# Optimization experiments

Hardware: AMD Instinct MI355X
Metric: run time of the kernel (lower is better)

The kernel has to match this reference:

```python
import jax, jax.numpy as jnp
import numpy as np
from jax import lax


def _lstm(x, h, c, W, U, b):
    # torch LSTM gate order: i, f, g, o; b = b_ih + b_hh combined
    g = x @ W.T + h @ U.T + b
    i, f, gg, o = jnp.split(g, 4, axis=-1)
    c2 = jax.nn.sigmoid(f) * c + jax.nn.sigmoid(i) * jnp.tanh(gg)
    h2 = jax.nn.sigmoid(o) * jnp.tanh(c2)
    return h2, c2


def _run_dir(x, mask, W, U, b):
    # packed-sequence semantics: state updates only where mask, outputs 0 at pad
    B = x.shape[0]
    Hh = U.shape[1]
    h0 = jnp.zeros((B, Hh), x.dtype)

    def step(carry, inp):
        h, c = carry
        xt, mt = inp
        h2, c2 = _lstm(xt, h, c, W, U, b)
        m = mt[:, None]
        h = jnp.where(m, h2, h)
        c = jnp.where(m, c2, c)
        return (h, c), jnp.where(m, h, jnp.zeros_like(h))

    (hf, cf), outs = lax.scan(step, (h0, h0), (jnp.swapaxes(x, 0, 1), mask.T))
    return jnp.swapaxes(outs, 0, 1), hf, cf  # (B,S,H), (B,H), (B,H)


def _forward(source, source_mask, target, target_mask, emb_src, emb_tgt,
             eW0f, eU0f, eb0f, eW0b, eU0b, eb0b,
             eW1f, eU1f, eb1f, eW1b, eU1b, eb1b,
             dW0, dU0, db0, dW1, dU1, db1, wW, wb):
    x = emb_src[source]  # (B,S,D)
    finals_h, finals_c = [], []
    enc_params = [(eW0f, eU0f, eb0f, eW0b, eU0b, eb0b),
                  (eW1f, eU1f, eb1f, eW1b, eU1b, eb1b)]
    for Wf, Uf, bf, Wb, Ub, bb in enc_params:
        of, hf, cf = _run_dir(x, source_mask, Wf, Uf, bf)
        # backward direction: reverse time; prefix mask becomes suffix, so the
        # masked-update scan exactly reproduces packed reverse-direction LSTM
        ob, hb, cb = _run_dir(x[:, ::-1], source_mask[:, ::-1], Wb, Ub, bb)
        ob = ob[:, ::-1]
        x = jnp.concatenate([of, ob], axis=-1)
        finals_h.append(jnp.concatenate([hf, hb], axis=-1))  # (B, 2H)
        finals_c.append(jnp.concatenate([cf, cb], axis=-1))

    # decoder initial state: per-layer concat of fwd/bwd encoder final states
    xt = emb_tgt[target]  # (B,T,D)

    def dstep(carry, inp):
        h1, c1, h2, c2 = carry
        t, mt = inp
        m = mt[:, None]
        nh1, nc1 = _lstm(t, h1, c1, dW0, dU0, db0)
        h1 = jnp.where(m, nh1, h1)
        c1 = jnp.where(m, nc1, c1)
        nh2, nc2 = _lstm(h1, h2, c2, dW1, dU1, db1)
        h2 = jnp.where(m, nh2, h2)
        c2 = jnp.where(m, nc2, c2)
        return (h1, c1, h2, c2), jnp.where(m, h2, jnp.zeros_like(h2))

    init = (finals_h[0], finals_c[0], finals_h[1], finals_c[1])
    _, outs = lax.scan(dstep, init, (jnp.swapaxes(xt, 0, 1), target_mask.T))
    outs = jnp.swapaxes(outs, 0, 1)  # (B,T,d_out)
    return jnp.einsum('btd,vd->btv', outs, wW) + wb  # (B,T,V)


def setup_inputs() -> dict:
    key = jax.random.key(0)
    ks = jax.random.split(key, 32)
    B, S, T, V, D, H = 32, 64, 65, 32000, 256, 512
    DO = 2 * H

    def p(i, shape):
        return jax.random.normal(ks[i], shape, dtype=jnp.float32) * 0.05

    source = jax.random.randint(ks[0], (B, S), 0, V + 1)
    target = jax.random.randint(ks[1], (B, T), 0, V + 1)
    # descending-sorted lengths -> sort/perm in the original is identity
    slen = jnp.sort(jax.random.randint(ks[2], (B,), 1, S + 1))[::-1]
    tlen = jnp.sort(jax.random.randint(ks[3], (B,), 1, T + 1))[::-1]
    source_mask = jnp.arange(S)[None, :] < slen[:, None]
    target_mask = jnp.arange(T)[None, :] < tlen[:, None]
    emb = p(4, (V + 1, D))
    return dict(
        source=source, source_mask=source_mask, target=target, target_mask=target_mask,
        emb_src=emb, emb_tgt=emb + 0.0,
        eW0f=p(5, (4 * H, D)), eU0f=p(6, (4 * H, H)), eb0f=p(7, (4 * H,)),
        eW0b=p(8, (4 * H, D)), eU0b=p(9, (4 * H, H)), eb0b=p(10, (4 * H,)),
        eW1f=p(11, (4 * H, 2 * H)), eU1f=p(12, (4 * H, H)), eb1f=p(13, (4 * H,)),
        eW1b=p(14, (4 * H, 2 * H)), eU1b=p(15, (4 * H, H)), eb1b=p(16, (4 * H,)),
        dW0=p(17, (4 * DO, D)), dU0=p(18, (4 * DO, DO)), db0=p(19, (4 * DO,)),
        dW1=p(20, (4 * DO, DO)), dU1=p(21, (4 * DO, DO)), db1=p(22, (4 * DO,)),
        wW=p(23, (V, DO)), wb=p(24, (V,)))


def reference(source, source_mask, target, target_mask, emb_src, emb_tgt,
              eW0f, eU0f, eb0f, eW0b, eU0b, eb0b,
              eW1f, eU1f, eb1f, eW1b, eU1b, eb1b,
              dW0, dU0, db0, dW1, dU1, db1, wW, wb):
    return _forward(source, source_mask, target, target_mask, emb_src, emb_tgt,
                    eW0f, eU0f, eb0f, eW0b, eU0b, eb0b,
                    eW1f, eU1f, eb1f, eW1b, eU1b, eb1b,
                    dW0, dU0, db0, dW1, dU1, db1, wW, wb)
```

## Files before the change

### kernel.cpp

```cpp
#include <hip/hip_runtime.h>

#define B_ 32
#define S_ 64
#define T_ 65
#define D_ 256
#define HE 512
#define HD 1024
#define VV 32000

typedef __attribute__((ext_vector_type(8))) short bf16x8;
typedef __attribute__((ext_vector_type(4))) float f32x4;
typedef __attribute__((ext_vector_type(4))) unsigned int u32x4;

__device__ inline unsigned short f2bf(float f) {
  unsigned int u = __float_as_uint(f);
  u += 0x7FFFu + ((u >> 16) & 1u);
  return (unsigned short)(u >> 16);
}
__device__ inline float sigmf(float x) { return 1.0f / (1.0f + __expf(-x)); }

#define MFMA16(a,b,c) __builtin_amdgcn_mfma_f32_16x16x32_bf16((a),(b),(c),0,0,0)

#define SLOT_STRIDE 32
__device__ inline void gbar_all(int* slots, int nblk, int e, int bid) {
  asm volatile("s_waitcnt vmcnt(0)" ::: "memory");
  __syncthreads();
  const int tid = threadIdx.x;
  if (tid == 0)
    __hip_atomic_store(&slots[bid * SLOT_STRIDE], e, __ATOMIC_RELAXED,
                       __HIP_MEMORY_SCOPE_AGENT);
  if (tid < nblk) {
    while (__hip_atomic_load(&slots[tid * SLOT_STRIDE], __ATOMIC_RELAXED,
                             __HIP_MEMORY_SCOPE_AGENT) < e)
      __builtin_amdgcn_s_sleep(2);
  }
  __syncthreads();
}

__device__ inline u32x4 ld16_sc(const void* p) {
  u32x4 r;
  asm volatile("global_load_dwordx4 %0, %1, off sc1"
               : "=v"(r)
               : "v"((unsigned long long)p)
               : "memory");
  return r;
}

__device__ inline int swz(int row, int col, int LD) {
  return row * LD + ((((col >> 3) ^ (row & 7)) << 3) | (col & 7));
}
template <int LD>
__device__ inline void stage1a(short* lds, const short* src) {
  const int tid = threadIdx.x;
  constexpr int NPT = LD / 64;
  u32x4 t[NPT];
#pragma unroll
  for (int i = 0; i < NPT; i++)
    t[i] = ld16_sc(src + ((size_t)(i * 256 + tid)) * 8);
  asm volatile("s_waitcnt vmcnt(0)" ::: "memory");
  __builtin_amdgcn_sched_barrier(0);
#pragma unroll
  for (int i = 0; i < NPT; i++) {
    int o = (i * 256 + tid) * 8;
    *(u32x4*)(lds + swz(o / LD, o % LD, LD)) = t[i];
  }
}
__device__ inline void stage2a(short* lds1, const short* s1, short* lds2,
                               const short* s2) {
  const int tid = threadIdx.x;
#pragma unroll
  for (int h = 0; h < 2; h++) {
    u32x4 a[8], b[8];
#pragma unroll
    for (int i = 0; i < 8; i++)
      a[i] = ld16_sc(s1 + ((size_t)((h * 8 + i) * 256 + tid)) * 8);
#pragma unroll
    for (int i = 0; i < 8; i++)
      b[i] = ld16_sc(s2 + ((size_t)((h * 8 + i) * 256 + tid)) * 8);
    asm volatile("s_waitcnt vmcnt(0)" ::: "memory");
    __builtin_amdgcn_sched_barrier(0);
#pragma unroll
    for (int i = 0; i < 8; i++) {
      int o = ((h * 8 + i) * 256 + tid) * 8;
      *(u32x4*)(lds1 + swz(o / HD, o % HD, HD)) = a[i];
    }
#pragma unroll
    for (int i = 0; i < 8; i++) {
      int o = ((h * 8 + i) * 256 + tid) * 8;
      *(u32x4*)(lds2 + swz(o / HD, o % HD, HD)) = b[i];
    }
  }
}

__device__ inline int mask_dtype(const unsigned char* m) {
  unsigned b0 = m[0], b1 = m[1], b2 = m[2], b3 = m[3], b4 = m[4];
  if (b0 == 1 && b1 == 1) return 0;
  if (b0 == 1) {
    if (b4 == 1) return 1;
    if (b4 == 0 && m[8] == 1) return 2;
    return 1;
  }
  if (b0 == 0x80 && b1 == 0x3F) return 4;
  if (b0 == 0x00 && b1 == 0x3C) return 5;
  if (b2 == 0x80 && b3 == 0x3F) return 3;
  return 1;
}
__device__ inline int mask_val(const unsigned char* m, int dt, int i) {
  switch (dt) {
    case 0: return m[i] != 0;
    case 1: return ((const int*)m)[i] != 0;
    case 2: return ((const long long*)m)[i] != 0;
    case 3: return ((const float*)m)[i] != 0.0f;
    default: return ((const unsigned short*)m)[i] != 0;
  }
}
__global__ void k_masks(const unsigned char* msrc, const unsigned char* mtgt,
                        signed char* o_src, signed char* o_tgt) {
  const unsigned char* m = blockIdx.x ? mtgt : msrc;
  signed char* o = blockIdx.x ? o_tgt : o_src;
  int n = blockIdx.x ? (B_ * T_) : (B_ * S_);
  int dt = mask_dtype(m);
  for (int i = threadIdx.x; i < n; i += blockDim.x)
    o[i] = (signed char)mask_val(m, dt, i);
}

struct CvtJobs {
  const float* src[13];
  short* dst[13];
  int n4[13];
};
__global__ __launch_bounds__(256) void k_convert(CvtJobs jb) {
  int j = blockIdx.y;
  const float4* s = (const float4*)jb.src[j];
  ushort4* d = (ushort4*)jb.dst[j];
  int n4 = jb.n4[j];
  for (int i = blockIdx.x * blockDim.x + threadIdx.x; i < n4;
       i += gridDim.x * blockDim.x) {
    float4 v = s[i];
    ushort4 o;
    o.x = f2bf(v.x); o.y = f2bf(v.y); o.z = f2bf(v.z); o.w = f2bf(v.w);
    d[i] = o;
  }
}

__global__ __launch_bounds__(256) void k_gather(const int* sids, const int* tids,
                                                const float* es, const float* et,
                                                short* Xs, short* Xt) {
  int job = blockIdx.y;
  int rows = job ? (B_ * T_) : (B_ * S_);
  const int* ids = job ? tids : sids;
  const float* emb = job ? et : es;
  ushort4* X = (ushort4*)(job ? Xt : Xs);
  int total = rows * (D_ / 4);
  for (int i = blockIdx.x * blockDim.x + threadIdx.x; i < total;
       i += gridDim.x * blockDim.x) {
    int row = i >> 6;
    int c4 = i & 63;
    long id = ids[row];
    float4 v = ((const float4*)(emb + id * (long)D_))[c4];
    ushort4 o;
    o.x = f2bf(v.x); o.y = f2bf(v.y); o.z = f2bf(v.z); o.w = f2bf(v.w);
    X[(long)row * 64 + c4] = o;
  }
}

template <bool B_F32, bool C_F32>
__global__ __launch_bounds__(256) void k_gemm(const short* __restrict__ A,
                                              const short* __restrict__ Bw,
                                              const float* __restrict__ Bwf,
                                              const float* __restrict__ bias,
                                              short* __restrict__ C,
                                              float* __restrict__ Cf,
                                              int M_out, int N, int K) {
  __shared__ short As[128 * 32];
  __shared__ short Bs[128 * 32];
  const int tid = threadIdx.x;
  const int wave = tid >> 6, lane = tid & 63;
  const int wm = wave >> 1, wn = wave & 1;
  const int r16 = lane & 15, kb = lane >> 4;
  const long m0 = (long)blockIdx.y * 128;
  const long n0 = (long)blockIdx.x * 128;

  const int ch0 = tid * 2, ch1 = ch0 + 1;
  const int ar0 = ch0 >> 2, ak0 = (ch0 & 3) * 8;
  const int ar1 = ch1 >> 2, ak1 = (ch1 & 3) * 8;

  f32x4 acc[4][4];
#pragma unroll
  for (int i = 0; i < 4; i++)
#pragma unroll
    for (int j = 0; j < 4; j++) acc[i][j] = (f32x4){0.f, 0.f, 0.f, 0.f};

  for (int kt = 0; kt < K; kt += 32) {
    bf16x8 va0 = *(const bf16x8*)(A + (m0 + ar0) * K + kt + ak0);
    bf16x8 va1 = *(const bf16x8*)(A + (m0 + ar1) * K + kt + ak1);
    bf16x8 vb0, vb1;
    if (B_F32) {
      const float* p0 = Bwf + (n0 + ar0) * K + kt + ak0;
      const float* p1 = Bwf + (n0 + ar1) * K + kt + ak1;
      float4 x0 = *(const float4*)p0, x1 = *(const float4*)(p0 + 4);
      float4 y0 = *(const float4*)p1, y1 = *(const float4*)(p1 + 4);
      vb0 = (bf16x8){(short)f2bf(x0.x), (short)f2bf(x0.y), (short)f2bf(x0.z),
                     (short)f2bf(x0.w), (short)f2bf(x1.x), (short)f2bf(x1.y),
                     (short)f2bf(x1.z), (short)f2bf(x1.w)};
      vb1 = (bf16x8){(short)f2bf(y0.x), (short)f2bf(y0.y), (short)f2bf(y0.z),
                     (short)f2bf(y0.w), (short)f2bf(y1.x), (short)f2bf(y1.y),
                     (short)f2bf(y1.z), (short)f2bf(y1.w)};
    } else {
      vb0 = *(const bf16x8*)(Bw + (n0 + ar0) * K + kt + ak0);
      vb1 = *(const bf16x8*)(Bw + (n0 + ar1) * K + kt + ak1);
    }
    __syncthreads();
    *(bf16x8*)(As + ar0 * 32 + ak0) = va0;
    *(bf16x8*)(As + ar1 * 32 + ak1) = va1;
    *(bf16x8*)(Bs + ar0 * 32 + ak0) = vb0;
    *(bf16x8*)(Bs + ar1 * 32 + ak1) = vb1;
    __syncthreads();
    bf16x8 av[4], bv[4];
#pragma unroll
    for (int i = 0; i < 4; i++)
      av[i] = *(const bf16x8*)(As + (wm * 64 + i * 16 + r16) * 32 + kb * 8);
#pragma unroll
    for (int j = 0; j < 4; j++)
      bv[j] = *(const bf16x8*)(Bs + (wn * 64 + j * 16 + r16) * 32 + kb * 8);
#pragma unroll
    for (int i = 0; i < 4; i++)
#pragma unroll
      for (int j = 0; j < 4; j++) acc[i][j] = MFMA16(av[i], bv[j], acc[i][j]);
  }
#pragma unroll
  for (int j = 0; j < 4; j++) {
    long gc = n0 + wn * 64 + j * 16 + r16;
    float bb = bias ? bias[gc] : 0.f;
#pragma unroll
    for (int i = 0; i < 4; i++) {
      long gr0 = m0 + wm * 64 + i * 16 + kb * 4;
#pragma unroll
      for (int r = 0; r < 4; r++) {
        long gr = gr0 + r;
        if (gr < M_out) {
          if (C_F32) Cf[gr * N + gc] = acc[i][j][r] + bb;
          else C[gr * N + gc] = (short)f2bf(acc[i][j][r] + bb);
        }
      }
    }
  }
}

__global__ __launch_bounds__(256) void k_enc_persist(
    const short* __restrict__ Wf, const short* __restrict__ Wb_,
    short* __restrict__ H, const float* __restrict__ Pf,
    const float* __restrict__ Pb, short* __restrict__ Outb, int outLD,
    int outOffDir, float* __restrict__ Cfin,
    const signed char* __restrict__ msk, int* slots) {
  const int dir = blockIdx.y;
  const short* W = dir ? Wb_ : Wf;
  const float* P = dir ? Pb : Pf;
  int* slotsD = slots + dir * 32 * SLOT_STRIDE;
  const int q = threadIdx.x >> 6, lane = threadIdx.x & 63;
  const int r16 = lane & 15, kb = lane >> 4;
  const int n = q * HE + blockIdx.x * 16 + r16;
  const short* wr = W + (size_t)n * HE;
  const int bb = threadIdx.x >> 3;
  const int cp = threadIdx.x & 7;
  const int j0 = blockIdx.x * 16 + 2 * cp;
  __shared__ short h_lds[32 * HE];
  __shared__ float g_lds[4][2][16][17];
  float creg0 = 0.f, creg1 = 0.f;

  for (int s = 0; s < S_; ++s) {
    const int t = dir ? (S_ - 1 - s) : s;
    const int rp = s & 1;
    const short* Ar = H + ((size_t)rp * 2 + dir) * (B_ * HE);
    short* Hw = H + ((size_t)(rp ^ 1) * 2 + dir) * (B_ * HE);

    const float* pr = P + (size_t)(bb * S_ + t) * (4 * HE);
    float2 pv[4];
#pragma unroll
    for (int g = 0; g < 4; g++) pv[g] = *(const float2*)(pr + g * HE + j0);
    bool valid = msk[bb * S_ + t] != 0;

    __syncthreads();
    stage1a<HE>(h_lds, Ar);
    __syncthreads();

    f32x4 acc0 = (f32x4){0.f, 0.f, 0.f, 0.f};
    f32x4 acc1 = (f32x4){0.f, 0.f, 0.f, 0.f};
#pragma unroll 8
    for (int k = kb * 8; k < HE; k += 32) {
      bf16x8 bv = *(const bf16x8*)(wr + k);
      bf16x8 a0 = *(const bf16x8*)(h_lds + swz(r16, k, HE));
      bf16x8 a1 = *(const bf16x8*)(h_lds + swz(16 + r16, k, HE));
      acc0 = MFMA16(a0, bv, acc0);
      acc1 = MFMA16(a1, bv, acc1);
    }
#pragma unroll
    for (int r = 0; r < 4; r++) {
      g_lds[q][0][kb * 4 + r][r16] = acc0[r];
      g_lds[q][1][kb * 4 + r][r16] = acc1[r];
    }
    __syncthreads();
    {
      const int mt = bb >> 4, br = bb & 15;
      float h2v[2];
#pragma unroll
      for (int cc = 0; cc < 2; ++cc) {
        float g0 = g_lds[0][mt][br][2 * cp + cc] + (cc ? pv[0].y : pv[0].x);
        float g1 = g_lds[1][mt][br][2 * cp + cc] + (cc ? pv[1].y : pv[1].x);
        float g2 = g_lds[2][mt][br][2 * cp + cc] + (cc ? pv[2].y : pv[2].x);
        float g3 = g_lds[3][mt][br][2 * cp + cc] + (cc ? pv[3].y : pv[3].x);
        float co = cc ? creg1 : creg0;
        float c2 = sigmf(g1) * co + sigmf(g0) * tanhf(g2);
        float h2 = sigmf(g3) * tanhf(c2);
        if (valid) { if (cc) creg1 = c2; else creg0 = c2; }
        h2v[cc] = h2;
      }
      unsigned short o0 = valid ? f2bf(h2v[0])
                                : (unsigned short)h_lds[swz(bb, j0, HE)];
      unsigned short o1 = valid ? f2bf(h2v[1])
                                : (unsigned short)h_lds[swz(bb, j0 + 1, HE)];
      unsigned int hv = (unsigned int)o0 | ((unsigned int)o1 << 16);
      __hip_atomic_store((unsigned int*)(Hw + bb * HE + j0), hv,
                         __ATOMIC_RELAXED, __HIP_MEMORY_SCOPE_AGENT);
      if (Outb) {
        unsigned int ov = valid ? hv : 0u;
        *(unsigned int*)(Outb + (size_t)(bb * S_ + t) * outLD +
                         outOffDir * dir + j0) = ov;
      }
    }
    if (s < S_ - 1) gbar_all(slotsD, 32, s + 1, blockIdx.x);
  }
  Cfin[(size_t)(dir * B_ + bb) * HE + j0] = creg0;
  Cfin[(size_t)(dir * B_ + bb) * HE + j0 + 1] = creg1;
}

__global__ __launch_bounds__(256) void k_dec_persist(
    const short* __restrict__ dU0b, const short* __restrict__ dW1b,
    const short* __restrict__ dU1b, short* __restrict__ H1,
    short* __restrict__ H2, const float* __restrict__ Q0,
    const float* __restrict__ db1f, const float* __restrict__ dC1i,
    const float* __restrict__ dC2i, short* __restrict__ douts,
    const signed char* __restrict__ msk, int* slots) {
  const int role = blockIdx.y;
  const int bid = role * 64 + blockIdx.x;
  const int q = threadIdx.x >> 6, lane = threadIdx.x & 63;
  const int r16 = lane & 15, kb = lane >> 4;
  const int n = q * HD + blockIdx.x * 16 + r16;
  const int bb = threadIdx.x >> 3;
  const int cp = threadIdx.x & 7;
  const int j0 = blockIdx.x * 16 + 2 * cp;
  __shared__ short h_lds1[32 * HD];
  __shared__ short h_lds2[32 * HD];
  __shared__ float g_lds[4][2][16][17];
  const float* Ci = role ? dC2i : dC1i;
  float creg0 = Ci[(size_t)bb * HD + j0];
  float creg1 = Ci[(size_t)bb * HD + j0 + 1];
  const short* w0 = dU0b + (size_t)n * HD;
  const short* w1 = dW1b + (size_t)n * HD;
  const short* w2 = dU1b + (size_t)n * HD;

  for (int k = 0; k <= T_; ++k) {
    if (role == 0 && k <= T_ - 1) {
      const int t = k, rp = k & 1;
      const short* Ar = H1 + (size_t)rp * (B_ * HD);
      short* Hw = H1 + (size_t)(rp ^ 1) * (B_ * HD);
      const float* pr = Q0 + (size_t)(bb * T_ + t) * (4 * HD);
      float2 pv[4];
#pragma unroll
      for (int g = 0; g < 4; g++) pv[g] = *(const float2*)(pr + g * HD + j0);
      bool valid = msk[bb * T_ + t] != 0;
      __syncthreads();
      stage1a<HD>(h_lds1, Ar);
      __syncthreads();
      f32x4 acc0 = (f32x4){0.f, 0.f, 0.f, 0.f};
      f32x4 acc1 = (f32x4){0.f, 0.f, 0.f, 0.f};
#pragma unroll 8
      for (int kk = kb * 8; kk < HD; kk += 32) {
        bf16x8 bv = *(const bf16x8*)(w0 + kk);
        bf16x8 a0 = *(const bf16x8*)(h_lds1 + swz(r16, kk, HD));
        bf16x8 a1 = *(const bf16x8*)(h_lds1 + swz(16 + r16, kk, HD));
        acc0 = MFMA16(a0, bv, acc0);
        acc1 = MFMA16(a1, bv, acc1);
      }
#pragma unroll
      for (int r = 0; r < 4; r++) {
        g_lds[q][0][kb * 4 + r][r16] = acc0[r];
        g_lds[q][1][kb * 4 + r][r16] = acc1[r];
      }
      __syncthreads();
      {
        const int mt = bb >> 4, br = bb & 15;
        float h2v[2];
#pragma unroll
        for (int cc = 0; cc < 2; ++cc) {
          float g0 = g_lds[0][mt][br][2 * cp + cc] + (cc ? pv[0].y : pv[0].x);
          float g1 = g_lds[1][mt][br][2 * cp + cc] + (cc ? pv[1].y : pv[1].x);
          float g2 = g_lds[2][mt][br][2 * cp + cc] + (cc ? pv[2].y : pv[2].x);
          float g3 = g_lds[3][mt][br][2 * cp + cc] + (cc ? pv[3].y : pv[3].x);
          float co = cc ? creg1 : creg0;
          float c2 = sigmf(g1) * co + sigmf(g0) * tanhf(g2);
          float h2 = sigmf(g3) * tanhf(c2);
          if (valid) { if (cc) creg1 = c2; else creg0 = c2; }
          h2v[cc] = h2;
        }
        unsigned short o0 = valid ? f2bf(h2v[0])
                                  : (unsigned short)h_lds1[swz(bb, j0, HD)];
        unsigned short o1 = valid ? f2bf(h2v[1])
                                  : (unsigned short)h_lds1[swz(bb, j0 + 1, HD)];
        unsigned int hv = (unsigned int)o0 | ((unsigned int)o1 << 16);
        __hip_atomic_store((unsigned int*)(Hw + bb * HD + j0), hv,
                           __ATOMIC_RELAXED, __HIP_MEMORY_SCOPE_AGENT);
      }
    } else if (role == 1 && k >= 1) {
      const int t = k - 1, rp = t & 1;
      const short* X = H1 + (size_t)(k & 1) * (B_ * HD);
      const short* Ar2 = H2 + (size_t)rp * (B_ * HD);
      short* Hw = H2 + (size_t)(rp ^ 1) * (B_ * HD);
      float2 pv[4];
#pragma unroll
      for (int g = 0; g < 4; g++) pv[g] = *(const float2*)(db1f + g * HD + j0);
      bool valid = msk[bb * T_ + t] != 0;
      __syncthreads();
      stage2a(h_lds1, X, h_lds2, Ar2);
      __syncthreads();
      f32x4 acc0 = (f32x4){0.f, 0.f, 0.f, 0.f};
      f32x4 acc1 = (f32x4){0.f, 0.f, 0.f, 0.f};
#pragma unroll 4
      for (int kk = kb * 8; kk < HD; kk += 32) {
        bf16x8 bv1 = *(const bf16x8*)(w1 + kk);
        bf16x8 a0 = *(const bf16x8*)(h_lds1 + swz(r16, kk, HD));
        bf16x8 a1 = *(const bf16x8*)(h_lds1 + swz(16 + r16, kk, HD));
        acc0 = MFMA16(a0, bv1, acc0);
        acc1 = MFMA16(a1, bv1, acc1);
        bf16x8 bv2 = *(const bf16x8*)(w2 + kk);
        bf16x8 b0 = *(const bf16x8*)(h_lds2 + swz(r16, kk, HD));
        bf16x8 b1 = *(const bf16x8*)(h_lds2 + swz(16 + r16, kk, HD));
        acc0 = MFMA16(b0, bv2, acc0);
        acc1 = MFMA16(b1, bv2, acc1);
      }
#pragma unroll
      for (int r = 0; r < 4; r++) {
        g_lds[q][0][kb * 4 + r][r16] = acc0[r];
        g_lds[q][1][kb * 4 + r][r16] = acc1[r];
      }
      __syncthreads();
      {
        const int mt = bb >> 4, br = bb & 15;
        float h2v[2];
#pragma unroll
        for (int cc = 0; cc < 2; ++cc) {
          float g0 = g_lds[0][mt][br][2 * cp + cc] + (cc ? pv[0].y : pv[0].x);
          float g1 = g_lds[1][mt][br][2 * cp + cc] + (cc ? pv[1].y : pv[1].x);
          float g2 = g_lds[2][mt][br][2 * cp + cc] + (cc ? pv[2].y : pv[2].x);
          float g3 = g_lds[3][mt][br][2 * cp + cc] + (cc ? pv[3].y : pv[3].x);
          float co = cc ? creg1 : creg0;
          float c2 = sigmf(g1) * co + sigmf(g0) * tanhf(g2);
          float h2 = sigmf(g3) * tanhf(c2);
          if (valid) { if (cc) creg1 = c2; else creg0 = c2; }
          h2v[cc] = h2;
        }
        unsigned short o0 = valid ? f2bf(h2v[0])
                                  : (unsigned short)h_lds2[swz(bb, j0, HD)];
        unsigned short o1 = valid ? f2bf(h2v[1])
                                  : (unsigned short)h_lds2[swz(bb, j0 + 1, HD)];
        unsigned int hv = (unsigned int)o0 | ((unsigned int)o1 << 16);
        __hip_atomic_store((unsigned int*)(Hw + bb * HD + j0), hv,
                           __ATOMIC_RELAXED, __HIP_MEMORY_SCOPE_AGENT);
        *(unsigned int*)(douts + (size_t)(bb * T_ + t) * HD + j0) =
            valid ? hv : 0u;
      }
    }
    if (k < T_) gbar_all(slots, 128, k + 1, bid);
  }
}

__global__ __launch_bounds__(256) void k_decinit(const short* h0, const float* c0,
                                                 const short* h1, const float* c1f,
                                                 short* dh1, float* dc1,
                                                 short* dh2, float* dc2) {
  int i = blockIdx.x * 256 + threadIdx.x;
  if (i < B_ * HD) {
    int b = i >> 10, nn = i & 1023, d = nn >> 9, jj = nn & 511;
    int src = (d * B_ + b) * HE + jj;
    dh1[i] = h0[src];
    dc1[i] = c0[src];
    dh2[i] = h1[src];
    dc2[i] = c1f[src];
  }
}

extern "C" void kernel_launch(void* const* d_in, const int* in_sizes, int n_in,
                              void* d_out, int out_size, void* d_ws, size_t ws_size,
                              hipStream_t stream) {
  const int* src = (const int*)d_in[0];
  const unsigned char* msrc = (const unsigned char*)d_in[1];
  const int* tgt = (const int*)d_in[2];
  const unsigned char* mtgt = (const unsigned char*)d_in[3];
  const float* emb_s = (const float*)d_in[4];
  const float* emb_t = (const float*)d_in[5];
  const float* eW0f = (const float*)d_in[6];
  const float* eU0f = (const float*)d_in[7];
  const float* eb0f = (const float*)d_in[8];
  const float* eW0b = (const float*)d_in[9];
  const float* eU0b = (const float*)d_in[10];
  const float* eb0b = (const float*)d_in[11];
  const float* eW1f = (const float*)d_in[12];
  const float* eU1f = (const float*)d_in[13];
  const float* eb1f = (const float*)d_in[14];
  const float* eW1b = (const float*)d_in[15];
  const float* eU1b = (const float*)d_in[16];
  const float* eb1b = (const float*)d_in[17];
  const float* dW0 = (const float*)d_in[18];
  const float* dU0 = (const float*)d_in[19];
  const float* db0 = (const float*)d_in[20];
  const float* dW1 = (const float*)d_in[21];
  const float* dU1 = (const float*)d_in[22];
  const float* db1 = (const float*)d_in[23];
  const float* wW = (const float*)d_in[24];
  const float* wb = (const float*)d_in[25];
  (void)n_in; (void)in_sizes; (void)out_size; (void)ws_size;

  short* douts = (short*)d_ws;
  short* wW_b = (short*)((char*)d_ws + (size_t)2176 * 1024 * 2);

  char* po = (char*)d_out;
  size_t off = 0;
  auto alloc = [&](size_t bytes) -> char* {
    char* p = po + off;
    off += (bytes + 255) & ~(size_t)255;
    return p;
  };
  const size_t szW[12] = {
      (size_t)2048 * 256 * 2,  (size_t)2048 * 512 * 2,
      (size_t)2048 * 256 * 2,  (size_t)2048 * 512 * 2,
      (size_t)2048 * 1024 * 2, (size_t)2048 * 512 * 2,
      (size_t)2048 * 1024 * 2, (size_t)2048 * 512 * 2,
      (size_t)4096 * 256 * 2,  (size_t)4096 * 1024 * 2,
      (size_t)4096 * 1024 * 2, (size_t)4096 * 1024 * 2};
  short* Wb[12];
  for (int i = 0; i < 12; i++) Wb[i] = (short*)alloc(szW[i]);
  short* eW0f_b = Wb[0], *eU0f_b = Wb[1], *eW0b_b = Wb[2], *eU0b_b = Wb[3];
  short* eW1f_b = Wb[4], *eU1f_b = Wb[5], *eW1b_b = Wb[6], *eU1b_b = Wb[7];
  short* dW0_b = Wb[8], *dU0_b = Wb[9], *dW1_b = Wb[10], *dU1_b = Wb[11];
  short* Xs_b = (short*)alloc((size_t)2048 * 256 * 2);
  short* Xt_b = (short*)alloc((size_t)2176 * 256 * 2);
  short* X1_b = (short*)alloc((size_t)2048 * 1024 * 2);
  char* uni = alloc((size_t)2176 * 4096 * 4);
  float* P0f = (float*)uni;
  float* P0b = P0f + (size_t)2048 * 2048;
  float* P1f = (float*)uni;
  float* P1b = P1f + (size_t)2048 * 2048;
  float* Q0 = (float*)uni;
  char* zero_begin = po + off;
  int* slots_e0 = (int*)alloc(2 * 32 * SLOT_STRIDE * 4);
  int* slots_e1 = (int*)alloc(2 * 32 * SLOT_STRIDE * 4);
  int* slots_d = (int*)alloc(128 * SLOT_STRIDE * 4);
  short* encH0 = (short*)alloc((size_t)2 * 2 * B_ * HE * 2);
  short* encH1 = (short*)alloc((size_t)2 * 2 * B_ * HE * 2);
  size_t zero_bytes = (size_t)((po + off) - zero_begin);
  float* Cfin0 = (float*)alloc((size_t)2 * B_ * HE * 4);
  float* Cfin1 = (float*)alloc((size_t)2 * B_ * HE * 4);
  short* dH1 = (short*)alloc((size_t)2 * B_ * HD * 2);
  short* dH2 = (short*)alloc((size_t)2 * B_ * HD * 2);
  float* dC1f = (float*)alloc((size_t)B_ * HD * 4);
  float* dC2f = (float*)alloc((size_t)B_ * HD * 4);
  signed char* msk_s = (signed char*)alloc(B_ * S_);
  signed char* msk_t = (signed char*)alloc(B_ * T_);

  const float* FN = nullptr;

  (void)hipMemsetAsync(douts, 0, (size_t)2176 * 1024 * 2, stream);
  (void)hipMemsetAsync(zero_begin, 0, zero_bytes, stream);
  k_masks<<<dim3(2), dim3(256), 0, stream>>>(msrc, mtgt, msk_s, msk_t);
  CvtJobs jb;
  const float* srcs[13] = {eW0f, eU0f, eW0b, eU0b, eW1f, eU1f,
                           eW1b, eU1b, dW0, dU0, dW1, dU1, wW};
  short* dsts[13] = {Wb[0], Wb[1], Wb[2], Wb[3], Wb[4], Wb[5],
                     Wb[6], Wb[7], Wb[8], Wb[9], Wb[10], Wb[11], wW_b};
  int ns[13] = {2048 * 256, 2048 * 512, 2048 * 256, 2048 * 512,
                2048 * 1024, 2048 * 512, 2048 * 1024, 2048 * 512,
                4096 * 256, 4096 * 1024, 4096 * 1024, 4096 * 1024, VV * 1024};
  for (int i = 0; i < 13; i++) { jb.src[i] = srcs[i]; jb.dst[i] = dsts[i]; jb.n4[i] = ns[i] / 4; }
  k_convert<<<dim3(1024, 13), 256, 0, stream>>>(jb);
  k_gather<<<dim3(544, 2), 256, 0, stream>>>(src, tgt, emb_s, emb_t, Xs_b, Xt_b);

  k_gemm<false, true><<<dim3(16, 16), 256, 0, stream>>>(
      Xs_b, eW0f_b, FN, eb0f, (short*)nullptr, P0f, 2048, 2048, 256);
  k_gemm<false, true><<<dim3(16, 16), 256, 0, stream>>>(
      Xs_b, eW0b_b, FN, eb0b, (short*)nullptr, P0b, 2048, 2048, 256);

  k_enc_persist<<<dim3(32, 2), 256, 0, stream>>>(
      eU0f_b, eU0b_b, encH0, P0f, P0b, X1_b, 1024, 512, Cfin0, msk_s, slots_e0);

  k_gemm<false, true><<<dim3(16, 16), 256, 0, stream>>>(
      X1_b, eW1f_b, FN, eb1f, (short*)nullptr, P1f, 2048, 2048, 1024);
  k_gemm<false, true><<<dim3(16, 16), 256, 0, stream>>>(
      X1_b, eW1b_b, FN, eb1b, (short*)nullptr, P1b, 2048, 2048, 1024);

  k_enc_persist<<<dim3(32, 2), 256, 0, stream>>>(
      eU1f_b, eU1b_b, encH1, P1f, P1b, (short*)nullptr, 0, 0, Cfin1, msk_s,
      slots_e1);

  k_decinit<<<dim3(128), 256, 0, stream>>>(encH0, Cfin0, encH1, Cfin1,
                                           dH1, dC1f, dH2, dC2f);

  k_gemm<false, true><<<dim3(32, 17), 256, 0, stream>>>(
      Xt_b, dW0_b, FN, db0, (short*)nullptr, Q0, 2176, 4096, 256);

  k_dec_persist<<<dim3(64, 2), 256, 0, stream>>>(
      dU0_b, dW1_b, dU1_b, dH1, dH2, Q0, db1, dC1f, dC2f, douts, msk_t,
      slots_d);

  k_gemm<false, true><<<dim3(250, 17), 256, 0, stream>>>(
      douts, wW_b, FN, wb, (short*)nullptr, (float*)d_out, B_ * T_, VV, 1024);
}
```

Baseline: 1.947 ms.

## Load GEMM tiles directly to LDS and overlap stage2a copies

The tiled GEMM now stages A and B tiles straight from global memory into LDS with global_load_lds, skipping the register round trip. The unused fp32-weight and bf16-output template paths are removed. In the recurrent kernels' staging helper, all 32 loads for both matrices are issued up front and the first matrix is written to LDS after a partial vmcnt wait, so the second matrix's loads overlap those writes. This raises register pressure in stage2a, and the GEMM's LDS layout now depends on the per-wave ordering of the direct loads.

Measured after the change: 1.903 ms. 1.02x faster.

```diff
diff --git a/kernel.cpp b/kernel.cpp
--- a/kernel.cpp
+++ b/kernel.cpp
@@ -46,6 +46,12 @@
   return r;
 }
 
+__device__ inline void gl_lds16(const short* g, short* l) {
+  __builtin_amdgcn_global_load_lds(
+      (const __attribute__((address_space(1))) short*)g,
+      (__attribute__((address_space(3))) short*)l, 16, 0, 0);
+}
+
 __device__ inline int swz(int row, int col, int LD) {
   return row * LD + ((((col >> 3) ^ (row & 7)) << 3) | (col & 7));
 }
@@ -68,27 +74,26 @@
 __device__ inline void stage2a(short* lds1, const short* s1, short* lds2,
                                const short* s2) {
   const int tid = threadIdx.x;
-#pragma unroll
-  for (int h = 0; h < 2; h++) {
-    u32x4 a[8], b[8];
-#pragma unroll
-    for (int i = 0; i < 8; i++)
-      a[i] = ld16_sc(s1 + ((size_t)((h * 8 + i) * 256 + tid)) * 8);
-#pragma unroll
-    for (int i = 0; i < 8; i++)
-      b[i] = ld16_sc(s2 + ((size_t)((h * 8 + i) * 256 + tid)) * 8);
-    asm volatile("s_waitcnt vmcnt(0)" ::: "memory");
-    __builtin_amdgcn_sched_barrier(0);
-#pragma unroll
-    for (int i = 0; i < 8; i++) {
-      int o = ((h * 8 + i) * 256 + tid) * 8;
-      *(u32x4*)(lds1 + swz(o / HD, o % HD, HD)) = a[i];
-    }
-#pragma unroll
-    for (int i = 0; i < 8; i++) {
-      int o = ((h * 8 + i) * 256 + tid) * 8;
-      *(u32x4*)(lds2 + swz(o / HD, o % HD, HD)) = b[i];
-    }
+  u32x4 t1[16], t2[16];
+#pragma unroll
+  for (int i = 0; i < 16; i++)
+    t1[i] = ld16_sc(s1 + ((size_t)(i * 256 + tid)) * 8);
+#pragma unroll
+  for (int i = 0; i < 16; i++)
+    t2[i] = ld16_sc(s2 + ((size_t)(i * 256 + tid)) * 8);
+  asm volatile("s_waitcnt vmcnt(16)" ::: "memory");
+  __builtin_amdgcn_sched_barrier(0);
+#pragma unroll
+  for (int i = 0; i < 16; i++) {
+    int o = (i * 256 + tid) * 8;
+    *(u32x4*)(lds1 + swz(o / HD, o % HD, HD)) = t1[i];
+  }
+  asm volatile("s_waitcnt vmcnt(0)" ::: "memory");
+  __builtin_amdgcn_sched_barrier(0);
+#pragma unroll
+  for (int i = 0; i < 16; i++) {
+    int o = (i * 256 + tid) * 8;
+    *(u32x4*)(lds2 + swz(o / HD, o % HD, HD)) = t2[i];
   }
 }
 
@@ -164,12 +169,9 @@
   }
 }
 
-template <bool B_F32, bool C_F32>
 __global__ __launch_bounds__(256) void k_gemm(const short* __restrict__ A,
                                               const short* __restrict__ Bw,
-                                              const float* __restrict__ Bwf,
                                               const float* __restrict__ bias,
-                                              short* __restrict__ C,
                                               float* __restrict__ Cf,
                                               int M_out, int N, int K) {
   __shared__ short As[128 * 32];
@@ -181,9 +183,13 @@
   const long m0 = (long)blockIdx.y * 128;
   const long n0 = (long)blockIdx.x * 128;
 
-  const int ch0 = tid * 2, ch1 = ch0 + 1;
-  const int ar0 = ch0 >> 2, ak0 = (ch0 & 3) * 8;
-  const int ar1 = ch1 >> 2, ak1 = (ch1 & 3) * 8;
+  const int c0 = wave * 128 + lane, c1 = c0 + 64;
+  const int rA0 = c0 >> 2, kA0 = (c0 & 3) * 8;
+  const int rA1 = c1 >> 2, kA1 = (c1 & 3) * 8;
+  short* lA0 = As + (size_t)(wave * 128) * 8;
+  short* lA1 = As + (size_t)(wave * 128 + 64) * 8;
+  short* lB0 = Bs + (size_t)(wave * 128) * 8;
+  short* lB1 = Bs + (size_t)(wave * 128 + 64) * 8;
 
   f32x4 acc[4][4];
 #pragma unroll
@@ -192,29 +198,11 @@
     for (int j = 0; j < 4; j++) acc[i][j] = (f32x4){0.f, 0.f, 0.f, 0.f};
 
   for (int kt = 0; kt < K; kt += 32) {
-    bf16x8 va0 = *(const bf16x8*)(A + (m0 + ar0) * K + kt + ak0);
-    bf16x8 va1 = *(const bf16x8*)(A + (m0 + ar1) * K + kt + ak1);
-    bf16x8 vb0, vb1;
-    if (B_F32) {
-      const float* p0 = Bwf + (n0 + ar0) * K + kt + ak0;
-      const float* p1 = Bwf + (n0 + ar1) * K + kt + ak1;
-      float4 x0 = *(const float4*)p0, x1 = *(const float4*)(p0 + 4);
-      float4 y0 = *(const float4*)p1, y1 = *(const float4*)(p1 + 4);
-      vb0 = (bf16x8){(short)f2bf(x0.x), (short)f2bf(x0.y), (short)f2bf(x0.z),
-                     (short)f2bf(x0.w), (short)f2bf(x1.x), (short)f2bf(x1.y),
-                     (short)f2bf(x1.z), (short)f2bf(x1.w)};
-      vb1 = (bf16x8){(short)f2bf(y0.x), (short)f2bf(y0.y), (short)f2bf(y0.z),
-                     (short)f2bf(y0.w), (short)f2bf(y1.x), (short)f2bf(y1.y),
-                     (short)f2bf(y1.z), (short)f2bf(y1.w)};
-    } else {
-      vb0 = *(const bf16x8*)(Bw + (n0 + ar0) * K + kt + ak0);
-      vb1 = *(const bf16x8*)(Bw + (n0 + ar1) * K + kt + ak1);
-    }
     __syncthreads();
-    *(bf16x8*)(As + ar0 * 32 + ak0) = va0;
-    *(bf16x8*)(As + ar1 * 32 + ak1) = va1;
-    *(bf16x8*)(Bs + ar0 * 32 + ak0) = vb0;
-    *(bf16x8*)(Bs + ar1 * 32 + ak1) = vb1;
+    gl_lds16(A + (m0 + rA0) * K + kt + kA0, lA0);
+    gl_lds16(A + (m0 + rA1) * K + kt + kA1, lA1);
+    gl_lds16(Bw + (n0 + rA0) * K + kt + kA0, lB0);
+    gl_lds16(Bw + (n0 + rA1) * K + kt + kA1, lB1);
     __syncthreads();
     bf16x8 av[4], bv[4];
 #pragma unroll
@@ -238,10 +226,7 @@
 #pragma unroll
       for (int r = 0; r < 4; r++) {
         long gr = gr0 + r;
-        if (gr < M_out) {
-          if (C_F32) Cf[gr * N + gc] = acc[i][j][r] + bb;
-          else C[gr * N + gc] = (short)f2bf(acc[i][j][r] + bb);
-        }
+        if (gr < M_out) Cf[gr * N + gc] = acc[i][j][r] + bb;
       }
     }
   }
@@ -567,8 +552,6 @@
   signed char* msk_s = (signed char*)alloc(B_ * S_);
   signed char* msk_t = (signed char*)alloc(B_ * T_);
 
-  const float* FN = nullptr;
-
   (void)hipMemsetAsync(douts, 0, (size_t)2176 * 1024 * 2, stream);
   (void)hipMemsetAsync(zero_begin, 0, zero_bytes, stream);
   k_masks<<<dim3(2), dim3(256), 0, stream>>>(msrc, mtgt, msk_s, msk_t);
@@ -584,18 +567,18 @@
   k_convert<<<dim3(1024, 13), 256, 0, stream>>>(jb);
   k_gather<<<dim3(544, 2), 256, 0, stream>>>(src, tgt, emb_s, emb_t, Xs_b, Xt_b);
 
-  k_gemm<false, true><<<dim3(16, 16), 256, 0, stream>>>(
-      Xs_b, eW0f_b, FN, eb0f, (short*)nullptr, P0f, 2048, 2048, 256);
-  k_gemm<false, true><<<dim3(16, 16), 256, 0, stream>>>(
-      Xs_b, eW0b_b, FN, eb0b, (short*)nullptr, P0b, 2048, 2048, 256);
+  k_gemm<<<dim3(16, 16), 256, 0, stream>>>(Xs_b, eW0f_b, eb0f, P0f,
+                                           2048, 2048, 256);
+  k_gemm<<<dim3(16, 16), 256, 0, stream>>>(Xs_b, eW0b_b, eb0b, P0b,
+                                           2048, 2048, 256);
 
   k_enc_persist<<<dim3(32, 2), 256, 0, stream>>>(
       eU0f_b, eU0b_b, encH0, P0f, P0b, X1_b, 1024, 512, Cfin0, msk_s, slots_e0);
 
-  k_gemm<false, true><<<dim3(16, 16), 256, 0, stream>>>(
-      X1_b, eW1f_b, FN, eb1f, (short*)nullptr, P1f, 2048, 2048, 1024);
-  k_gemm<false, true><<<dim3(16, 16), 256, 0, stream>>>(
-      X1_b, eW1b_b, FN, eb1b, (short*)nullptr, P1b, 2048, 2048, 1024);
+  k_gemm<<<dim3(16, 16), 256, 0, stream>>>(X1_b, eW1f_b, eb1f, P1f,
+                                           2048, 2048, 1024);
+  k_gemm<<<dim3(16, 16), 256, 0, stream>>>(X1_b, eW1b_b, eb1b, P1b,
+                                           2048, 2048, 1024);
 
   k_enc_persist<<<dim3(32, 2), 256, 0, stream>>>(
       eU1f_b, eU1b_b, encH1, P1f, P1b, (short*)nullptr, 0, 0, Cfin1, msk_s,
@@ -604,13 +587,13 @@
   k_decinit<<<dim3(128), 256, 0, stream>>>(encH0, Cfin0, encH1, Cfin1,
                                            dH1, dC1f, dH2, dC2f);
 
-  k_gemm<false, true><<<dim3(32, 17), 256, 0, stream>>>(
-      Xt_b, dW0_b, FN, db0, (short*)nullptr, Q0, 2176, 4096, 256);
+  k_gemm<<<dim3(32, 17), 256, 0, stream>>>(Xt_b, dW0_b, db0, Q0,
+                                           2176, 4096, 256);
 
   k_dec_persist<<<dim3(64, 2), 256, 0, stream>>>(
       dU0_b, dW1_b, dU1_b, dH1, dH2, Q0, db1, dC1f, dC2f, douts, msk_t,
       slots_d);
 
-  k_gemm<false, true><<<dim3(250, 17), 256, 0, stream>>>(
-      douts, wW_b, FN, wb, (short*)nullptr, (float*)d_out, B_ * T_, VV, 1024);
-}
+  k_gemm<<<dim3(250, 17), 256, 0, stream>>>(douts, wW_b, wb, (float*)d_out,
+                                            B_ * T_, VV, 1024);
+}
```
